# Performance work log

Measured on AMD Instinct MI355X. Metric: run time of the kernel, lower is better.

## Reference

```python
import jax, jax.numpy as jnp
import numpy as np

N = 6144
HIDDEN = 48
HEADS = 3
HEAD = HIDDEN // HEADS


def setup_inputs() -> dict:
    key = jax.random.key(0)
    ks = jax.random.split(key, 8)
    s = 1.0 / np.sqrt(HIDDEN)
    A = (jax.random.uniform(ks[0], (N, N)) < 0.05).astype(jnp.float32)
    h = jax.random.normal(ks[1], (N, HIDDEN), dtype=jnp.float32)
    Wq = jax.random.normal(ks[2], (HIDDEN, HIDDEN), dtype=jnp.float32) * s
    Wk = jax.random.normal(ks[3], (HIDDEN, HIDDEN), dtype=jnp.float32) * s
    Wv = jax.random.normal(ks[4], (HIDDEN, HIDDEN), dtype=jnp.float32) * s
    bq = jnp.zeros((HIDDEN,), jnp.float32)
    bk = jnp.zeros((HIDDEN,), jnp.float32)
    bv = jnp.zeros((HIDDEN,), jnp.float32)
    return {"A": A, "h": h, "Wq": Wq, "bq": bq, "Wk": Wk, "bk": bk, "Wv": Wv, "bv": bv}


def reference(A, h, Wq, bq, Wk, bk, Wv, bv):
    n = h.shape[0]
    # QKV projections (torch Linear: x @ W.T + b)
    q = (h @ Wq.T + bq).reshape(n, HEADS, HEAD).transpose(1, 0, 2)  # [H,N,d]
    k = (h @ Wk.T + bk).reshape(n, HEADS, HEAD).transpose(1, 0, 2)
    v = (h @ Wv.T + bv).reshape(n, HEADS, HEAD).transpose(1, 0, 2)
    # scores = (q k^T) * A / N**(-0.5)  == (q k^T) * A * sqrt(N)  (faithful to source)
    scale = jnp.asarray(n, h.dtype) ** 0.5
    scores = jnp.einsum("hnd,hmd->hnm", q, k) * A[None, :, :] * scale
    scores = jax.nn.softmax(scores, axis=2)
    out = jnp.einsum("hnm,hmd->hnd", scores, v)  # [H,N,d]
    out = out.transpose(1, 0, 2).reshape(n, HIDDEN)
    return (out, scores)
```

## Files before the change

kernel.cpp:

```cpp
#include <hip/hip_runtime.h>
#include <math.h>

#define NN   6144
#define HID  48
#define BLK  512
#define RPB  4
#define CAP  448
#define CTOT (RPB*CAP)
#define SCALE 78.38367176906175f

typedef float vf4 __attribute__((ext_vector_type(4)));

__global__ __launch_bounds__(256)
void qkv_kernel(const float* __restrict__ h,
                const float* __restrict__ Wq, const float* __restrict__ bq,
                const float* __restrict__ Wk, const float* __restrict__ bk,
                const float* __restrict__ Wv, const float* __restrict__ bv,
                float* __restrict__ qw, float* __restrict__ kw, float* __restrict__ vw) {
    int idx = blockIdx.x * blockDim.x + threadIdx.x;
    int i = idx / HID, c = idx % HID;
    const float4* h4  = (const float4*)(h + (size_t)i * HID);
    const float4* wq4 = (const float4*)(Wq + (size_t)c * HID);
    const float4* wk4 = (const float4*)(Wk + (size_t)c * HID);
    const float4* wv4 = (const float4*)(Wv + (size_t)c * HID);
    float aq = 0.f, ak = 0.f, av = 0.f;
    #pragma unroll
    for (int r = 0; r < HID / 4; ++r) {
        float4 hv = h4[r];
        float4 q4 = wq4[r], k4 = wk4[r], v4 = wv4[r];
        aq = fmaf(hv.x, q4.x, aq); aq = fmaf(hv.y, q4.y, aq);
        aq = fmaf(hv.z, q4.z, aq); aq = fmaf(hv.w, q4.w, aq);
        ak = fmaf(hv.x, k4.x, ak); ak = fmaf(hv.y, k4.y, ak);
        ak = fmaf(hv.z, k4.z, ak); ak = fmaf(hv.w, k4.w, ak);
        av = fmaf(hv.x, v4.x, av); av = fmaf(hv.y, v4.y, av);
        av = fmaf(hv.w, v4.w, av); av = fmaf(hv.z, v4.z, av);
    }
    aq += bq[c]; ak += bk[c]; av += bv[c];
    int head = c >> 4, d = c & 15;
    size_t off = ((size_t)head * NN + i) * 16 + d;
    qw[off] = aq; kw[off] = ak; vw[off] = av;
}

__global__ __launch_bounds__(256)
void vtot_kernel(const float* __restrict__ vw, float* __restrict__ vtot) {
    int c = blockIdx.x;
    int head = c >> 4, d = c & 15;
    float s = 0.f;
    for (int j = threadIdx.x; j < NN; j += 256)
        s += vw[((size_t)head * NN + j) * 16 + d];
    #pragma unroll
    for (int o = 32; o; o >>= 1) s += __shfl_xor(s, o, 64);
    __shared__ float red[4];
    int wid = threadIdx.x >> 6, lane = threadIdx.x & 63;
    if (lane == 0) red[wid] = s;
    __syncthreads();
    if (threadIdx.x == 0) vtot[c] = red[0] + red[1] + red[2] + red[3];
}

__global__ __launch_bounds__(BLK)
void attn_kernel(const float* __restrict__ A,
                 const float* __restrict__ qw, const float* __restrict__ kw,
                 const float* __restrict__ vw, const float* __restrict__ vtot,
                 float* __restrict__ out) {
    __shared__ int   list[CTOT];
    __shared__ float sc[3][CTOT];
    __shared__ __align__(16) float qs[RPB * 48];
    __shared__ unsigned pm[RPB][BLK];
    __shared__ float wredML[8 * 12 * 2];
    __shared__ float MF[12], ZF[12], IVF[12];
    __shared__ unsigned wlo[8], whi[8];

    const int i0 = blockIdx.x * RPB;
    const int tid = threadIdx.x;
    const int wid = tid >> 6, lane = tid & 63;

    if (tid < RPB * 48) {
        int r = tid / 48, c = tid % 48;
        int hh = c >> 4, d = c & 15;
        qs[tid] = qw[((size_t)hh * NN + (i0 + r)) * 16 + d];
    }

    unsigned long long amask = 0ull;
    #pragma unroll
    for (int r = 0; r < RPB; ++r) {
        const vf4* Ar = (const vf4*)(A + (size_t)(i0 + r) * NN);
        #pragma unroll
        for (int c = 0; c < 3; ++c) {
            vf4 a4 = __builtin_nontemporal_load(&Ar[tid + c * BLK]);
            int p = r * 16 + c * 4;
            if (a4.x != 0.f) amask |= 1ull << (p + 0);
            if (a4.y != 0.f) amask |= 1ull << (p + 1);
            if (a4.z != 0.f) amask |= 1ull << (p + 2);
            if (a4.w != 0.f) amask |= 1ull << (p + 3);
        }
    }
    unsigned m0 = (unsigned)(amask & 0xFFFull);
    unsigned m1 = (unsigned)((amask >> 16) & 0xFFFull);
    unsigned m2 = (unsigned)((amask >> 32) & 0xFFFull);
    unsigned m3 = (unsigned)((amask >> 48) & 0xFFFull);
    unsigned lo = (unsigned)__popc(m0) | ((unsigned)__popc(m1) << 16);
    unsigned hi = (unsigned)__popc(m2) | ((unsigned)__popc(m3) << 16);

    unsigned ilo = lo, ihi = hi;
    #pragma unroll
    for (int o = 1; o < 64; o <<= 1) {
        unsigned plo = __shfl_up(ilo, o, 64);
        unsigned phi = __shfl_up(ihi, o, 64);
        if (lane >= o) { ilo += plo; ihi += phi; }
    }
    if (lane == 63) { wlo[wid] = ilo; whi[wid] = ihi; }
    __syncthreads();
    unsigned blo = ilo - lo, bhi = ihi - hi;
    unsigned tlo = 0, thi = 0;
    #pragma unroll
    for (int w = 0; w < 8; ++w) {
        unsigned a = wlo[w], b = whi[w];
        if (w < wid) { blo += a; bhi += b; }
        tlo += a; thi += b;
    }
    const int C0 = min((int)(tlo & 0xFFFFu), CAP), C1 = min((int)(tlo >> 16), CAP);
    const int C2 = min((int)(thi & 0xFFFFu), CAP), C3 = min((int)(thi >> 16), CAP);
    const int cum1 = C0, cum2 = C0 + C1, cum3 = cum2 + C2;
    int bs[4] = {(int)(blo & 0xFFFFu), (int)(blo >> 16),
                 (int)(bhi & 0xFFFFu), (int)(bhi >> 16)};
    int cu[5] = {0, cum1, cum2, cum3, cum3 + C3};
    unsigned mr[4] = {m0, m1, m2, m3};

    #pragma unroll
    for (int r = 0; r < RPB; ++r)
        pm[r][tid] = mr[r] | ((unsigned)bs[r] << 12);

    #pragma unroll
    for (int r = 0; r < RPB; ++r) {
        unsigned m = mr[r];
        int b = bs[r];
        while (m) {
            int p = __ffs(m) - 1; m &= m - 1;
            if (b < CAP) list[cu[r] + b] = 4 * (tid + (p >> 2) * BLK) + (p & 3);
            ++b;
        }
    }
    __syncthreads();

    {
        const int q4 = tid >> 2, part = tid & 3;
        #pragma unroll
        for (int r = 0; r < RPB; ++r) {
            float4 qv0 = ((const float4*)(qs + r * 48 +  0))[part];
            float4 qv1 = ((const float4*)(qs + r * 48 + 16))[part];
            float4 qv2 = ((const float4*)(qs + r * 48 + 32))[part];
            float mA = 0.f, lA = 0.f, mB = 0.f, lB = 0.f, mC = 0.f, lC = 0.f;
            for (int e = cu[r] + q4; e < cu[r + 1]; e += (BLK >> 2)) {
                int j = list[e];
                float4 k0 = ((const float4*)(kw + ((size_t)0 * NN + j) * 16))[part];
                float4 k1 = ((const float4*)(kw + ((size_t)1 * NN + j) * 16))[part];
                float4 k2 = ((const float4*)(kw + ((size_t)2 * NN + j) * 16))[part];
                float d0 = k0.x * qv0.x; d0 = fmaf(k0.y, qv0.y, d0);
                d0 = fmaf(k0.z, qv0.z, d0); d0 = fmaf(k0.w, qv0.w, d0);
                float d1 = k1.x * qv1.x; d1 = fmaf(k1.y, qv1.y, d1);
                d1 = fmaf(k1.z, qv1.z, d1); d1 = fmaf(k1.w, qv1.w, d1);
                float d2 = k2.x * qv2.x; d2 = fmaf(k2.y, qv2.y, d2);
                d2 = fmaf(k2.z, qv2.z, d2); d2 = fmaf(k2.w, qv2.w, d2);
                d0 += __shfl_xor(d0, 1, 64); d0 += __shfl_xor(d0, 2, 64);
                d1 += __shfl_xor(d1, 1, 64); d1 += __shfl_xor(d1, 2, 64);
                d2 += __shfl_xor(d2, 1, 64); d2 += __shfl_xor(d2, 2, 64);
                float s0 = d0 * SCALE, s1 = d1 * SCALE, s2 = d2 * SCALE;
                if (part == 0) sc[0][e] = s0;
                else if (part == 1) sc[1][e] = s1;
                else if (part == 2) sc[2][e] = s2;
                float nm;
                nm = fmaxf(mA, s0); lA = lA * __expf(mA - nm) + __expf(s0 - nm); mA = nm;
                nm = fmaxf(mB, s1); lB = lB * __expf(mB - nm) + __expf(s1 - nm); mB = nm;
                nm = fmaxf(mC, s2); lC = lC * __expf(mC - nm) + __expf(s2 - nm); mC = nm;
            }
            #pragma unroll
            for (int o = 4; o < 64; o <<= 1) {
                float om, ol, nm;
                om = __shfl_xor(mA, o, 64); ol = __shfl_xor(lA, o, 64);
                nm = fmaxf(mA, om); lA = lA * __expf(mA - nm) + ol * __expf(om - nm); mA = nm;
                om = __shfl_xor(mB, o, 64); ol = __shfl_xor(lB, o, 64);
                nm = fmaxf(mB, om); lB = lB * __expf(mB - nm) + ol * __expf(om - nm); mB = nm;
                om = __shfl_xor(mC, o, 64); ol = __shfl_xor(lC, o, 64);
                nm = fmaxf(mC, om); lC = lC * __expf(mC - nm) + ol * __expf(om - nm); mC = nm;
            }
            if (lane == 0) {
                int b0 = (wid * 12 + r * 3) * 2;
                wredML[b0 + 0] = mA; wredML[b0 + 1] = lA;
                wredML[b0 + 2] = mB; wredML[b0 + 3] = lB;
                wredML[b0 + 4] = mC; wredML[b0 + 5] = lC;
            }
        }
    }
    __syncthreads();

    if (tid < 12) {
        int r = tid / 3;
        int Cr = (r == 0) ? C0 : (r == 1) ? C1 : (r == 2) ? C2 : C3;
        float M = wredML[tid * 2], L = wredML[tid * 2 + 1];
        #pragma unroll
        for (int w = 1; w < 8; ++w) {
            float mw = wredML[(w * 12 + tid) * 2], lw = wredML[(w * 12 + tid) * 2 + 1];
            float nm = fmaxf(M, mw);
            L = L * __expf(M - nm) + lw * __expf(mw - nm);
            M = nm;
        }
        float z = __expf(-M);
        MF[tid] = M; ZF[tid] = z;
        IVF[tid] = 1.0f / (L + (float)(NN - Cr) * z);
    }
    __syncthreads();

    if (wid < 3) {
        const int h = wid, rr4 = lane & 3, a = lane >> 2;
        const float* vbase = vw + (size_t)h * NN * 16 + rr4 * 4;
        #pragma unroll
        for (int r = 0; r < RPB; ++r) {
            int s = r * 3 + h;
            float M = MF[s], zz = ZF[s], iv = IVF[s];
            float ax = 0.f, ay = 0.f, az = 0.f, aw = 0.f;
            #pragma unroll 2
            for (int e = cu[r] + a; e < cu[r + 1]; e += 16) {
                float p = __expf(sc[h][e] - M);
                float w = p - zz;
                int j = list[e];
                float4 vv = *(const float4*)(vbase + (size_t)j * 16);
                ax = fmaf(w, vv.x, ax); ay = fmaf(w, vv.y, ay);
                az = fmaf(w, vv.z, az); aw = fmaf(w, vv.w, aw);
            }
            #pragma unroll
            for (int o = 4; o < 64; o <<= 1) {
                ax += __shfl_xor(ax, o, 64); ay += __shfl_xor(ay, o, 64);
                az += __shfl_xor(az, o, 64); aw += __shfl_xor(aw, o, 64);
            }
            if (a == 0) {
                int c0 = h * 16 + rr4 * 4;
                float4 vt = *(const float4*)(vtot + c0);
                float4 o4;
                o4.x = (ax + zz * vt.x) * iv;
                o4.y = (ay + zz * vt.y) * iv;
                o4.z = (az + zz * vt.z) * iv;
                o4.w = (aw + zz * vt.w) * iv;
                *(float4*)(out + (size_t)(i0 + r) * HID + c0) = o4;
            }
        }
    } else {
        float* Pp = out + (size_t)NN * HID;
        const size_t NSQ = (size_t)NN * NN;
        const int t = tid - 192;
        #pragma unroll
        for (int r = 0; r < RPB; ++r) {
            int s = r * 3;
            float M0 = MF[s], M1 = MF[s + 1], M2 = MF[s + 2];
            float iv0 = IVF[s], iv1 = IVF[s + 1], iv2 = IVF[s + 2];
            float zi0 = ZF[s] * iv0, zi1 = ZF[s + 1] * iv1, zi2 = ZF[s + 2] * iv2;
            size_t rowoff = (size_t)(i0 + r) * NN;
            #pragma unroll 2
            for (int p = t; p < NN / 4; p += 320) {
                unsigned pk = pm[r][p & (BLK - 1)];
                int c = p >> 9;
                unsigned msk = pk & 0xFFFu;
                unsigned nib = (msk >> (c * 4)) & 0xFu;
                int idx = (int)(pk >> 12) + __popc(msk & ((1u << (c * 4)) - 1u));
                vf4 P0, P1, P2;
                #pragma unroll
                for (int e = 0; e < 4; ++e) {
                    int nz = (int)((nib >> e) & 1u);
                    if (nz && idx < CAP) {
                        int slot = cu[r] + idx;
                        P0[e] = __expf(sc[0][slot] - M0) * iv0;
                        P1[e] = __expf(sc[1][slot] - M1) * iv1;
                        P2[e] = __expf(sc[2][slot] - M2) * iv2;
                    } else { P0[e] = zi0; P1[e] = zi1; P2[e] = zi2; }
                    idx += nz;
                }
                __builtin_nontemporal_store(P0, &((vf4*)(Pp + rowoff))[p]);
                __builtin_nontemporal_store(P1, &((vf4*)(Pp + NSQ + rowoff))[p]);
                __builtin_nontemporal_store(P2, &((vf4*)(Pp + 2 * NSQ + rowoff))[p]);
            }
        }
    }
}

extern "C" void kernel_launch(void* const* d_in, const int* in_sizes, int n_in,
                              void* d_out, int out_size, void* d_ws, size_t ws_size,
                              hipStream_t stream) {
    const float* A  = (const float*)d_in[0];
    const float* h  = (const float*)d_in[1];
    const float* Wq = (const float*)d_in[2];
    const float* bq = (const float*)d_in[3];
    const float* Wk = (const float*)d_in[4];
    const float* bk = (const float*)d_in[5];
    const float* Wv = (const float*)d_in[6];
    const float* bv = (const float*)d_in[7];
    float* out = (float*)d_out;
    float* ws  = (float*)d_ws;

    float* qw   = ws;
    float* kw   = ws + (size_t)3 * NN * 16;
    float* vw   = ws + (size_t)6 * NN * 16;
    float* vtot = ws + (size_t)9 * NN * 16;

    qkv_kernel<<<(NN * HID) / 256, 256, 0, stream>>>(h, Wq, bq, Wk, bk, Wv, bv, qw, kw, vw);
    vtot_kernel<<<HID, 256, 0, stream>>>(vw, vtot);
    attn_kernel<<<NN / RPB, BLK, 0, stream>>>(A, qw, kw, vw, vtot, out);
}
```

Before: 609.4 us.

## Split adjacency scan into a separate list-building kernel before attention

Moves the read of the dense adjacency matrix and the compaction of nonzero column indices into a new listbuild kernel that writes per-row index lists, packed masks and counts to workspace. The attention kernel then reads these compact lists instead of streaming the full A rows, which frees shared memory (the pm array) and adds a launch-bounds occupancy hint. The intent is to separate the memory-bound A scan from the compute-heavy attention phase and raise occupancy there. In exchange it adds a global round trip for the lists and masks (about 11 MB of extra traffic) and one more kernel launch.

Result: slower. 655.2 us (+7.5%).

```diff
diff --git a/kernel.cpp b/kernel.cpp
--- a/kernel.cpp
+++ b/kernel.cpp
@@ -58,27 +58,13 @@
 }
 
 __global__ __launch_bounds__(BLK)
-void attn_kernel(const float* __restrict__ A,
-                 const float* __restrict__ qw, const float* __restrict__ kw,
-                 const float* __restrict__ vw, const float* __restrict__ vtot,
-                 float* __restrict__ out) {
-    __shared__ int   list[CTOT];
-    __shared__ float sc[3][CTOT];
-    __shared__ __align__(16) float qs[RPB * 48];
-    __shared__ unsigned pm[RPB][BLK];
-    __shared__ float wredML[8 * 12 * 2];
-    __shared__ float MF[12], ZF[12], IVF[12];
+void listbuild_kernel(const float* __restrict__ A,
+                      int* __restrict__ listG, unsigned* __restrict__ pmG,
+                      int* __restrict__ cntG) {
     __shared__ unsigned wlo[8], whi[8];
-
     const int i0 = blockIdx.x * RPB;
     const int tid = threadIdx.x;
     const int wid = tid >> 6, lane = tid & 63;
-
-    if (tid < RPB * 48) {
-        int r = tid / 48, c = tid % 48;
-        int hh = c >> 4, d = c & 15;
-        qs[tid] = qw[((size_t)hh * NN + (i0 + r)) * 16 + d];
-    }
 
     unsigned long long amask = 0ull;
     #pragma unroll
@@ -120,26 +106,57 @@
     }
     const int C0 = min((int)(tlo & 0xFFFFu), CAP), C1 = min((int)(tlo >> 16), CAP);
     const int C2 = min((int)(thi & 0xFFFFu), CAP), C3 = min((int)(thi >> 16), CAP);
-    const int cum1 = C0, cum2 = C0 + C1, cum3 = cum2 + C2;
     int bs[4] = {(int)(blo & 0xFFFFu), (int)(blo >> 16),
                  (int)(bhi & 0xFFFFu), (int)(bhi >> 16)};
-    int cu[5] = {0, cum1, cum2, cum3, cum3 + C3};
     unsigned mr[4] = {m0, m1, m2, m3};
 
     #pragma unroll
-    for (int r = 0; r < RPB; ++r)
-        pm[r][tid] = mr[r] | ((unsigned)bs[r] << 12);
-
-    #pragma unroll
     for (int r = 0; r < RPB; ++r) {
+        __builtin_nontemporal_store(mr[r] | ((unsigned)bs[r] << 12),
+                                    &pmG[(size_t)(i0 + r) * BLK + tid]);
         unsigned m = mr[r];
         int b = bs[r];
         while (m) {
             int p = __ffs(m) - 1; m &= m - 1;
-            if (b < CAP) list[cu[r] + b] = 4 * (tid + (p >> 2) * BLK) + (p & 3);
+            if (b < CAP)
+                listG[(size_t)(i0 + r) * CAP + b] = 4 * (tid + (p >> 2) * BLK) + (p & 3);
             ++b;
         }
     }
+    if (tid < 4)
+        cntG[i0 + tid] = (tid == 0) ? C0 : (tid == 1) ? C1 : (tid == 2) ? C2 : C3;
+}
+
+__global__ __launch_bounds__(BLK, 4)
+void attn_kernel(const float* __restrict__ qw, const float* __restrict__ kw,
+                 const float* __restrict__ vw, const float* __restrict__ vtot,
+                 const int* __restrict__ listG, const unsigned* __restrict__ pmG,
+                 const int* __restrict__ cntG, float* __restrict__ out) {
+    __shared__ int   list[CTOT];
+    __shared__ float sc[3][CTOT];
+    __shared__ __align__(16) float qs[RPB * 48];
+    __shared__ float wredML[8 * 12 * 2];
+    __shared__ float MF[12], ZF[12], IVF[12];
+
+    const int i0 = blockIdx.x * RPB;
+    const int tid = threadIdx.x;
+    const int wid = tid >> 6, lane = tid & 63;
+
+    const int Cr0 = cntG[i0 + 0], Cr1 = cntG[i0 + 1];
+    const int Cr2 = cntG[i0 + 2], Cr3 = cntG[i0 + 3];
+    int Cr4[4] = {Cr0, Cr1, Cr2, Cr3};
+    int cu[5] = {0, Cr0, Cr0 + Cr1, Cr0 + Cr1 + Cr2, Cr0 + Cr1 + Cr2 + Cr3};
+
+    if (tid < RPB * 48) {
+        int r = tid / 48, c = tid % 48;
+        int hh = c >> 4, d = c & 15;
+        qs[tid] = qw[((size_t)hh * NN + (i0 + r)) * 16 + d];
+    }
+
+    #pragma unroll
+    for (int r = 0; r < RPB; ++r)
+        for (int idx = tid; idx < Cr4[r]; idx += BLK)
+            list[cu[r] + idx] = listG[(size_t)(i0 + r) * CAP + idx];
     __syncthreads();
 
     {
@@ -195,7 +212,7 @@
 
     if (tid < 12) {
         int r = tid / 3;
-        int Cr = (r == 0) ? C0 : (r == 1) ? C1 : (r == 2) ? C2 : C3;
+        int Cr = Cr4[r];
         float M = wredML[tid * 2], L = wredML[tid * 2 + 1];
         #pragma unroll
         for (int w = 1; w < 8; ++w) {
@@ -254,9 +271,10 @@
             float iv0 = IVF[s], iv1 = IVF[s + 1], iv2 = IVF[s + 2];
             float zi0 = ZF[s] * iv0, zi1 = ZF[s + 1] * iv1, zi2 = ZF[s + 2] * iv2;
             size_t rowoff = (size_t)(i0 + r) * NN;
+            const unsigned* pmrow = pmG + (size_t)(i0 + r) * BLK;
             #pragma unroll 2
             for (int p = t; p < NN / 4; p += 320) {
-                unsigned pk = pm[r][p & (BLK - 1)];
+                unsigned pk = pmrow[p & (BLK - 1)];
                 int c = p >> 9;
                 unsigned msk = pk & 0xFFFu;
                 unsigned nib = (msk >> (c * 4)) & 0xFu;
@@ -296,11 +314,15 @@
     float* ws  = (float*)d_ws;
 
     float* qw   = ws;
-    float* kw   = ws + (size_t)3 * NN * 16;
-    float* vw   = ws + (size_t)6 * NN * 16;
-    float* vtot = ws + (size_t)9 * NN * 16;
-
+    float* kw   = qw + (size_t)3 * NN * 16;
+    float* vw   = kw + (size_t)3 * NN * 16;
+    float* vtot = vw + (size_t)3 * NN * 16;
+    int*   cntG = (int*)(vtot + 64);
+    int*   listG = cntG + NN;
+    unsigned* pmG = (unsigned*)(listG + (size_t)NN * CAP);
+
+    listbuild_kernel<<<NN / RPB, BLK, 0, stream>>>(A, listG, pmG, cntG);
     qkv_kernel<<<(NN * HID) / 256, 256, 0, stream>>>(h, Wq, bq, Wk, bk, Wv, bv, qw, kw, vw);
     vtot_kernel<<<HID, 256, 0, stream>>>(vw, vtot);
-    attn_kernel<<<NN / RPB, BLK, 0, stream>>>(A, qw, kw, vw, vtot, out);
-}
+    attn_kernel<<<NN / RPB, BLK, 0, stream>>>(qw, kw, vw, vtot, listG, pmG, cntG, out);
+}
```
